# Kernel tuning notes

Measured on AMD Instinct MI355X. Metric: run time of the kernel, lower is better.

Reference implementation:

```python
import jax, jax.numpy as jnp
import numpy as np

C_S = 768
C_Z = 128
D = 32            # c_hidden (hardcoded in module)
H = C_S // D      # 24 heads
EPS = 1e-5
INF = 1e9


def setup_inputs() -> dict:
    key = jax.random.key(0)
    ks = jax.random.split(key, 16)
    B, S = 2, 1024
    n = lambda k, shp, s=1.0: jax.random.normal(k, shp, dtype=jnp.float32) * s
    return {
        "bs": n(ks[0], (B, S, C_S)),
        "z": n(ks[1], (S, S, C_Z)),
        "t": n(ks[2], (B, C_S)),
        "beta": n(ks[3], (B, S, S), 0.1),
        "z_mask": jax.random.randint(ks[4], (S, S), 0, 2).astype(jnp.int32),
        "w_adaln": n(ks[5], (C_S, 3 * C_S), 0.02),
        "b_adaln": n(ks[6], (3 * C_S,), 0.1),
        "ln_z_w": jnp.ones((C_Z,), jnp.float32),
        "ln_z_b": jnp.zeros((C_Z,), jnp.float32),
        "w_q": n(ks[7], (C_S, C_S), 0.02),
        "w_k": n(ks[8], (C_S, C_S), 0.02),
        "w_v": n(ks[9], (C_S, C_S), 0.02),
        "w_z": n(ks[10], (C_Z, H), 0.02),
        "rms_q_w": jnp.ones((D,), jnp.float32),
        "rms_k_w": jnp.ones((D,), jnp.float32),
        "w_o": n(ks[11], (C_S, C_S), 0.02),
        "b_o": jnp.zeros((C_S,), jnp.float32),
    }


def _ln(x, eps=EPS):
    mu = jnp.mean(x, axis=-1, keepdims=True)
    var = jnp.mean((x - mu) ** 2, axis=-1, keepdims=True)
    return (x - mu) * jax.lax.rsqrt(var + eps)


def _rms(x, w, eps=EPS):
    return x * jax.lax.rsqrt(jnp.mean(x * x, axis=-1, keepdims=True) + eps) * w


def reference(bs, z, t, beta, z_mask, w_adaln, b_adaln, ln_z_w, ln_z_b,
              w_q, w_k, w_v, w_z, rms_q_w, rms_k_w, w_o, b_o):
    B, S, _ = bs.shape
    # AdaLayerNormZero: SiLU(t) -> Linear -> (shift, scale, gate)
    emb = jax.nn.silu(t) @ w_adaln + b_adaln                # [B, 3*C_S]
    shift, scale, gate = jnp.split(emb, 3, axis=-1)
    bs_norm = _ln(bs) * (1.0 + scale[:, None, :]) + shift[:, None, :]
    gate = gate[:, None, :]                                  # [B,1,C_S]
    # LayerNorm on pair rep
    z_norm = _ln(z) * ln_z_w + ln_z_b                        # [S,S,C_Z]
    # Q/K/V with QK-RMSNorm
    q = _rms((bs_norm @ w_q).reshape(B, S, H, D).transpose(0, 2, 1, 3), rms_q_w)
    k = _rms((bs_norm @ w_k).reshape(B, S, H, D).transpose(0, 2, 1, 3), rms_k_w)
    v = (bs_norm @ w_v).reshape(B, S, H, D).transpose(0, 2, 1, 3)
    # pair bias [1,H,S,S] + mask bias + beta
    bias = jnp.einsum('ijc,ch->hij', z_norm, w_z)[None]
    mask_bias = jnp.where(z_mask.astype(jnp.float32) > 0.5, 0.0, -INF)[None, None]
    bias = bias + mask_bias + beta[:, None, :, :]
    scores = jnp.einsum('bhqd,bhkd->bhqk', q, k) * (1.0 / np.sqrt(D)) + bias
    attn = jax.nn.softmax(scores, axis=-1)
    out = jnp.einsum('bhqk,bhkd->bhqd', attn, v).transpose(0, 2, 1, 3).reshape(B, S, C_S)
    return (out @ w_o + b_o) * gate
```

## Files before the change

### kernel.cpp

```cpp
#include <hip/hip_runtime.h>
#include <hip/hip_bf16.h>
#include <math.h>

#define SQ 1024
#define CS 768
#define CZ 128
#define DD 32
#define NH 24
#define EPSV 1e-5f

typedef __hip_bfloat16 bf16;
typedef _Float16 f16;
typedef _Float16 f16x8 __attribute__((ext_vector_type(8)));
typedef float f32x4 __attribute__((ext_vector_type(4)));

__device__ __forceinline__ float b2f(bf16 x) { return __bfloat162float(x); }
__device__ __forceinline__ bf16 f2b(float x) { return __float2bfloat16(x); }

__global__ __launch_bounds__(256) void k_adaln(const float* t, const float* w,
                                               const float* bias, float* emb) {
    __shared__ float st[CS];
    int b = blockIdx.y;
    int o = blockIdx.x * 256 + threadIdx.x;
    for (int c = threadIdx.x; c < CS; c += 256) {
        float x = t[b * CS + c];
        st[c] = x / (1.0f + __expf(-x));
    }
    __syncthreads();
    float acc = bias[o];
    for (int c = 0; c < CS; ++c)
        acc += st[c] * w[(size_t)c * (3 * CS) + o];
    emb[(size_t)b * 3 * CS + o] = acc;
}

__global__ __launch_bounds__(256) void k_bsnorm(const float* bs, const float* emb,
                                                float* bsn) {
    int row = blockIdx.x;
    int b = row >> 10;
    const float* x = bs + (size_t)row * CS;
    float v[3], s1 = 0.f, s2 = 0.f;
    #pragma unroll
    for (int i = 0; i < 3; i++) {
        float f = x[threadIdx.x + i * 256];
        v[i] = f; s1 += f; s2 += f * f;
    }
    __shared__ float red[8];
    for (int off = 32; off; off >>= 1) { s1 += __shfl_down(s1, off); s2 += __shfl_down(s2, off); }
    int wid = threadIdx.x >> 6;
    if ((threadIdx.x & 63) == 0) { red[wid] = s1; red[wid + 4] = s2; }
    __syncthreads();
    s1 = red[0] + red[1] + red[2] + red[3];
    s2 = red[4] + red[5] + red[6] + red[7];
    float mu = s1 * (1.0f / CS);
    float var = s2 * (1.0f / CS) - mu * mu;
    float rs = rsqrtf(var + EPSV);
    const float* sh = emb + (size_t)b * 3 * CS;
    float* o = bsn + (size_t)row * CS;
    #pragma unroll
    for (int i = 0; i < 3; i++) {
        int c = threadIdx.x + i * 256;
        o[c] = (v[i] - mu) * rs * (1.0f + sh[CS + c]) + sh[c];
    }
}

__global__ __launch_bounds__(256) void k_gemm_qkv(const float* A, const float* W,
                                                  float* out) {
    __shared__ float As[16][68];
    __shared__ float Bs[16][68];
    int t = threadIdx.x;
    int m0g = blockIdx.x * 64;
    int n0g = blockIdx.y * 64;
    int mg = t >> 4, ng = t & 15;
    float acc[4][4] = {};
    for (int k0 = 0; k0 < CS; k0 += 16) {
        {
            int kk = t & 15, mm = t >> 4;
            #pragma unroll
            for (int r = 0; r < 4; r++)
                As[kk][mm + r * 16] = A[(size_t)(m0g + mm + r * 16) * CS + k0 + kk];
            int nn = (t & 15) * 4, kb = t >> 4;
            float4 w4 = *(const float4*)&W[(size_t)(k0 + kb) * CS + n0g + nn];
            *(float4*)&Bs[kb][nn] = w4;
        }
        __syncthreads();
        #pragma unroll
        for (int kk = 0; kk < 16; kk++) {
            float4 a4 = *(const float4*)&As[kk][mg * 4];
            float4 b4 = *(const float4*)&Bs[kk][ng * 4];
            float a[4] = {a4.x, a4.y, a4.z, a4.w};
            float bv[4] = {b4.x, b4.y, b4.z, b4.w};
            #pragma unroll
            for (int ii = 0; ii < 4; ii++)
                #pragma unroll
                for (int jj = 0; jj < 4; jj++)
                    acc[ii][jj] += a[ii] * bv[jj];
        }
        __syncthreads();
    }
    #pragma unroll
    for (int ii = 0; ii < 4; ii++) {
        int r = m0g + mg * 4 + ii;
        int b = r >> 10, s = r & 1023;
        #pragma unroll
        for (int jj = 0; jj < 4; jj++) {
            int c = n0g + ng * 4 + jj;
            int h = c >> 5, d = c & 31;
            out[(((size_t)b * NH + h) * SQ + s) * DD + d] = acc[ii][jj];
        }
    }
}

__global__ __launch_bounds__(256) void k_rms(float* x, const float* w) {
    int g = blockIdx.x * 8 + (threadIdx.x >> 5);
    int d = threadIdx.x & 31;
    float* p = x + (size_t)g * DD + d;
    float v = *p;
    float s = v * v;
    for (int off = 16; off; off >>= 1) s += __shfl_xor(s, off, 32);
    float rs = rsqrtf(s * (1.0f / DD) + EPSV);
    *p = v * rs * w[d];
}

__global__ __launch_bounds__(64) void k_uv(const float* wz, const float* lnw,
                                           const float* lnb, float* uv) {
    int t = threadIdx.x;
    if (t < 2 * NH) {
        int h = t % NH;
        const float* s = (t < NH) ? lnw : lnb;
        float a = 0.f;
        for (int c = 0; c < CZ; ++c) a += s[c] * wz[c * NH + h];
        uv[t] = a;
    }
}

#define ZROWS 64
#define ZSTRIDE 132
__global__ __launch_bounds__(256) void k_zbias(const float* z, const int* zmask,
                                               const float* wz, const float* lnw,
                                               const float* lnb, const float* uv,
                                               bf16* zbias) {
    __shared__ float zt[ZROWS * ZSTRIDE];
    __shared__ bf16 ot[NH][ZROWS];
    int t = threadIdx.x;
    size_t base = (size_t)blockIdx.x * ZROWS;
    const float4* src = (const float4*)(z + base * CZ);
    #pragma unroll
    for (int it = 0; it < 8; it++) {
        int gi = t + it * 256;
        int row = gi >> 5, c4 = gi & 31;
        int cs = (c4 * 4) ^ ((row >> 3) << 2);
        *(float4*)&zt[row * ZSTRIDE + cs] = src[gi];
    }
    __syncthreads();
    int lane = t & 63;
    int qd = __builtin_amdgcn_readfirstlane(t >> 6);
    int sw = (lane >> 3) << 2;
    float acc[NH];
    #pragma unroll
    for (int h = 0; h < NH; h++) acc[h] = 0.f;
    float s1 = 0.f, s2 = 0.f;
    #pragma unroll
    for (int i = 0; i < 8; i++) {
        int c0 = qd * 32 + i * 4;
        float4 zv = *(const float4*)&zt[lane * ZSTRIDE + (c0 ^ sw)];
        float e[4] = {zv.x, zv.y, zv.z, zv.w};
        #pragma unroll
        for (int u = 0; u < 4; u++) {
            int c = c0 + u;
            float zval = e[u];
            s1 += zval;
            s2 = fmaf(zval, zval, s2);
            float tc = zval * lnw[c];
            #pragma unroll
            for (int h = 0; h < NH; h++)
                acc[h] = fmaf(tc, wz[c * NH + h], acc[h]);
        }
    }
    __syncthreads();
    {
        float* pp = zt + qd * (ZROWS * 27) + lane * 27;
        pp[0] = s1; pp[1] = s2;
        #pragma unroll
        for (int h = 0; h < NH; h++) pp[2 + h] = acc[h];
    }
    __syncthreads();
    int r = lane;
    int hb = qd * 6;
    float fs1 = 0.f, fs2 = 0.f;
    float fa[6] = {};
    #pragma unroll
    for (int q = 0; q < 4; q++) {
        const float* p = zt + q * (ZROWS * 27) + r * 27;
        fs1 += p[0]; fs2 += p[1];
        #pragma unroll
        for (int j = 0; j < 6; j++) fa[j] += p[2 + hb + j];
    }
    float mu = fs1 * (1.0f / CZ);
    float var = fs2 * (1.0f / CZ) - mu * mu;
    float rs = rsqrtf(var + EPSV);
    float mb = (zmask[base + r] > 0) ? 0.0f : -1.0e9f;
    #pragma unroll
    for (int j = 0; j < 6; j++) {
        int h = hb + j;
        float val = rs * fa[j] - mu * rs * uv[h] + uv[NH + h] + mb;
        ot[h][r] = f2b(val);
    }
    __syncthreads();
    size_t SS = (size_t)SQ * SQ;
    if (t < 192) {
        int h = t >> 3, l8 = t & 7;
        uint4 val = *(const uint4*)&ot[h][l8 * 8];
        *(uint4*)&zbias[(size_t)h * SS + base + l8 * 8] = val;
    }
}

#define PQK 40
#define PPV 72
__global__ __launch_bounds__(256) void k_attn(const float* q, const float* k,
                                              const float* v, const bf16* zbias,
                                              const float* beta, float* attn_out) {
    int qt = blockIdx.x;
    int bh = blockIdx.y;
    int b = bh / NH, h = bh % NH;
    __shared__ f16 Qs[64 * PQK];
    __shared__ f16 Ks[64 * PQK];
    __shared__ f16 Vs[32 * PPV];
    __shared__ f16 Ps[64 * PPV];
    int t = threadIdx.x;
    int w = t >> 6, l = t & 63;
    int lg = l >> 4, ll = l & 15;
    const float scale = 0.17677669529663687f;
    size_t SS = (size_t)SQ * SQ;
    int srow = t >> 2, sc0 = (t & 3) * 8;

    {
        const float* qb = q + ((size_t)bh * SQ + qt * 64) * DD;
        float4 a0 = *(const float4*)&qb[srow * DD + sc0];
        float4 a1 = *(const float4*)&qb[srow * DD + sc0 + 4];
        f16x8 hv;
        hv[0] = (f16)(a0.x * scale); hv[1] = (f16)(a0.y * scale);
        hv[2] = (f16)(a0.z * scale); hv[3] = (f16)(a0.w * scale);
        hv[4] = (f16)(a1.x * scale); hv[5] = (f16)(a1.y * scale);
        hv[6] = (f16)(a1.z * scale); hv[7] = (f16)(a1.w * scale);
        *(f16x8*)&Qs[srow * PQK + sc0] = hv;
    }
    f32x4 accO0 = {0.f, 0.f, 0.f, 0.f}, accO1 = {0.f, 0.f, 0.f, 0.f};
    float m_reg[4], l_reg[4];
    #pragma unroll
    for (int r = 0; r < 4; r++) { m_reg[r] = -3.0e38f; l_reg[r] = 0.f; }

    float4 kr0, kr1, vr0, vr1;
    {
        const float* kb = k + ((size_t)bh * SQ) * DD;
        const float* vb = v + ((size_t)bh * SQ) * DD;
        kr0 = *(const float4*)&kb[srow * DD + sc0];
        kr1 = *(const float4*)&kb[srow * DD + sc0 + 4];
        vr0 = *(const float4*)&vb[srow * DD + sc0];
        vr1 = *(const float4*)&vb[srow * DD + sc0 + 4];
    }
    __syncthreads();
    {
        f16x8 hk;
        hk[0] = (f16)kr0.x; hk[1] = (f16)kr0.y; hk[2] = (f16)kr0.z; hk[3] = (f16)kr0.w;
        hk[4] = (f16)kr1.x; hk[5] = (f16)kr1.y; hk[6] = (f16)kr1.z; hk[7] = (f16)kr1.w;
        *(f16x8*)&Ks[srow * PQK + sc0] = hk;
        float vv[8] = {vr0.x, vr0.y, vr0.z, vr0.w, vr1.x, vr1.y, vr1.z, vr1.w};
        #pragma unroll
        for (int u = 0; u < 8; u++) Vs[(sc0 + u) * PPV + srow] = (f16)vv[u];
    }
    const unsigned short* zb = (const unsigned short*)(zbias + (size_t)h * SS);
    const float* bb = beta + (size_t)b * SS;
    int ibase = qt * 64 + w * 16 + lg * 4;

    for (int kt = 0; kt < 16; kt++) {
        __syncthreads();
        if (kt < 15) {
            const float* kb = k + ((size_t)bh * SQ + (kt + 1) * 64) * DD;
            const float* vb = v + ((size_t)bh * SQ + (kt + 1) * 64) * DD;
            kr0 = *(const float4*)&kb[srow * DD + sc0];
            kr1 = *(const float4*)&kb[srow * DD + sc0 + 4];
            vr0 = *(const float4*)&vb[srow * DD + sc0];
            vr1 = *(const float4*)&vb[srow * DD + sc0 + 4];
        }
        f32x4 acc[4];
        #pragma unroll
        for (int c = 0; c < 4; c++) {
            #pragma unroll
            for (int r = 0; r < 4; r++) {
                size_t off = (size_t)(ibase + r) * SQ + kt * 64 + c * 16 + ll;
                union { unsigned u; float f; } cv;
                cv.u = (unsigned)zb[off] << 16;
                acc[c][r] = cv.f + bb[off];
            }
        }
        f16x8 aQ = *(const f16x8*)&Qs[(w * 16 + ll) * PQK + lg * 8];
        #pragma unroll
        for (int c = 0; c < 4; c++) {
            f16x8 bK = *(const f16x8*)&Ks[(c * 16 + ll) * PQK + lg * 8];
            acc[c] = __builtin_amdgcn_mfma_f32_16x16x32_f16(aQ, bK, acc[c], 0, 0, 0);
        }
        float al[4];
        #pragma unroll
        for (int r = 0; r < 4; r++) {
            float mx = fmaxf(fmaxf(acc[0][r], acc[1][r]), fmaxf(acc[2][r], acc[3][r]));
            #pragma unroll
            for (int off = 1; off < 16; off <<= 1) mx = fmaxf(mx, __shfl_xor(mx, off, 64));
            float mn = fmaxf(m_reg[r], mx);
            al[r] = __expf(m_reg[r] - mn);
            float ps = 0.f;
            #pragma unroll
            for (int c = 0; c < 4; c++) {
                float p = __expf(acc[c][r] - mn);
                acc[c][r] = p;
                ps += p;
            }
            #pragma unroll
            for (int off = 1; off < 16; off <<= 1) ps += __shfl_xor(ps, off, 64);
            m_reg[r] = mn;
            l_reg[r] = l_reg[r] * al[r] + ps;
        }
        #pragma unroll
        for (int c = 0; c < 4; c++)
            #pragma unroll
            for (int r = 0; r < 4; r++)
                Ps[(w * 16 + lg * 4 + r) * PPV + c * 16 + ll] = (f16)acc[c][r];
        #pragma unroll
        for (int r = 0; r < 4; r++) { accO0[r] *= al[r]; accO1[r] *= al[r]; }
        __asm__ volatile("s_waitcnt lgkmcnt(0)" ::: "memory");
        #pragma unroll
        for (int jt = 0; jt < 2; jt++) {
            f16x8 aP = *(const f16x8*)&Ps[(w * 16 + ll) * PPV + jt * 32 + lg * 8];
            f16x8 bV0 = *(const f16x8*)&Vs[(ll) * PPV + jt * 32 + lg * 8];
            f16x8 bV1 = *(const f16x8*)&Vs[(16 + ll) * PPV + jt * 32 + lg * 8];
            accO0 = __builtin_amdgcn_mfma_f32_16x16x32_f16(aP, bV0, accO0, 0, 0, 0);
            accO1 = __builtin_amdgcn_mfma_f32_16x16x32_f16(aP, bV1, accO1, 0, 0, 0);
        }
        __syncthreads();
        if (kt < 15) {
            f16x8 hk;
            hk[0] = (f16)kr0.x; hk[1] = (f16)kr0.y; hk[2] = (f16)kr0.z; hk[3] = (f16)kr0.w;
            hk[4] = (f16)kr1.x; hk[5] = (f16)kr1.y; hk[6] = (f16)kr1.z; hk[7] = (f16)kr1.w;
            *(f16x8*)&Ks[srow * PQK + sc0] = hk;
            float vv[8] = {vr0.x, vr0.y, vr0.z, vr0.w, vr1.x, vr1.y, vr1.z, vr1.w};
            #pragma unroll
            for (int u = 0; u < 8; u++) Vs[(sc0 + u) * PPV + srow] = (f16)vv[u];
        }
    }
    #pragma unroll
    for (int r = 0; r < 4; r++) {
        float inv = 1.0f / l_reg[r];
        int row = qt * 64 + w * 16 + lg * 4 + r;
        float* op = attn_out + ((size_t)b * SQ + row) * CS + h * DD;
        op[ll] = accO0[r] * inv;
        op[16 + ll] = accO1[r] * inv;
    }
}

__global__ __launch_bounds__(256) void k_gemm_out(const float* A, const float* W,
                                                  const float* b_o, const float* emb,
                                                  float* out) {
    __shared__ float As[16][68];
    __shared__ float Bs[16][68];
    int t = threadIdx.x;
    int m0g = blockIdx.x * 64;
    int n0g = blockIdx.y * 64;
    int mg = t >> 4, ng = t & 15;
    float acc[4][4] = {};
    for (int k0 = 0; k0 < CS; k0 += 16) {
        {
            int kk = t & 15, mm = t >> 4;
            #pragma unroll
            for (int r = 0; r < 4; r++)
                As[kk][mm + r * 16] = A[(size_t)(m0g + mm + r * 16) * CS + k0 + kk];
            int nn = (t & 15) * 4, kb = t >> 4;
            float4 w4 = *(const float4*)&W[(size_t)(k0 + kb) * CS + n0g + nn];
            *(float4*)&Bs[kb][nn] = w4;
        }
        __syncthreads();
        #pragma unroll
        for (int kk = 0; kk < 16; kk++) {
            float4 a4 = *(const float4*)&As[kk][mg * 4];
            float4 b4 = *(const float4*)&Bs[kk][ng * 4];
            float a[4] = {a4.x, a4.y, a4.z, a4.w};
            float bv[4] = {b4.x, b4.y, b4.z, b4.w};
            #pragma unroll
            for (int ii = 0; ii < 4; ii++)
                #pragma unroll
                for (int jj = 0; jj < 4; jj++)
                    acc[ii][jj] += a[ii] * bv[jj];
        }
        __syncthreads();
    }
    #pragma unroll
    for (int ii = 0; ii < 4; ii++) {
        int r = m0g + mg * 4 + ii;
        int b = r >> 10;
        int c0 = n0g + ng * 4;
        const float* gt = emb + (size_t)b * 3 * CS + 2 * CS;
        float4 o4;
        o4.x = (acc[ii][0] + b_o[c0 + 0]) * gt[c0 + 0];
        o4.y = (acc[ii][1] + b_o[c0 + 1]) * gt[c0 + 1];
        o4.z = (acc[ii][2] + b_o[c0 + 2]) * gt[c0 + 2];
        o4.w = (acc[ii][3] + b_o[c0 + 3]) * gt[c0 + 3];
        *(float4*)&out[(size_t)r * CS + c0] = o4;
    }
}

extern "C" void kernel_launch(void* const* d_in, const int* in_sizes, int n_in,
                              void* d_out, int out_size, void* d_ws, size_t ws_size,
                              hipStream_t stream) {
    const float* bs      = (const float*)d_in[0];
    const float* z       = (const float*)d_in[1];
    const float* t       = (const float*)d_in[2];
    const float* beta    = (const float*)d_in[3];
    const int*   z_mask  = (const int*)d_in[4];
    const float* w_adaln = (const float*)d_in[5];
    const float* b_adaln = (const float*)d_in[6];
    const float* ln_z_w  = (const float*)d_in[7];
    const float* ln_z_b  = (const float*)d_in[8];
    const float* w_q     = (const float*)d_in[9];
    const float* w_k     = (const float*)d_in[10];
    const float* w_v     = (const float*)d_in[11];
    const float* w_z     = (const float*)d_in[12];
    const float* rms_q_w = (const float*)d_in[13];
    const float* rms_k_w = (const float*)d_in[14];
    const float* w_o     = (const float*)d_in[15];
    const float* b_o     = (const float*)d_in[16];
    float* out = (float*)d_out;

    char* ws = (char*)d_ws;
    const size_t SZ_QKV = (size_t)2 * SQ * CS * 4;
    float* emb   = (float*)(ws);
    float* bsn   = (float*)(ws + 32768);
    float* qbuf  = (float*)(ws + 32768 + SZ_QKV);
    float* kbuf  = (float*)(ws + 32768 + 2 * SZ_QKV);
    float* vbuf  = (float*)(ws + 32768 + 3 * SZ_QKV);
    float* attn  = (float*)(ws + 32768 + 4 * SZ_QKV);
    bf16*  zbias = (bf16*)(ws + 32768 + 5 * SZ_QKV);
    float* uv    = (float*)(ws + 32768 + 5 * SZ_QKV + 50331648);

    k_adaln<<<dim3(9, 2), 256, 0, stream>>>(t, w_adaln, b_adaln, emb);
    k_uv<<<1, 64, 0, stream>>>(w_z, ln_z_w, ln_z_b, uv);
    k_bsnorm<<<2048, 256, 0, stream>>>(bs, emb, bsn);
    k_gemm_qkv<<<dim3(32, 12), 256, 0, stream>>>(bsn, w_q, qbuf);
    k_gemm_qkv<<<dim3(32, 12), 256, 0, stream>>>(bsn, w_k, kbuf);
    k_gemm_qkv<<<dim3(32, 12), 256, 0, stream>>>(bsn, w_v, vbuf);
    k_rms<<<6144, 256, 0, stream>>>(qbuf, rms_q_w);
    k_rms<<<6144, 256, 0, stream>>>(kbuf, rms_k_w);
    k_zbias<<<16384, 256, 0, stream>>>(z, z_mask, w_z, ln_z_w, ln_z_b, uv, zbias);
    k_attn<<<dim3(16, 48), 256, 0, stream>>>(qbuf, kbuf, vbuf, zbias, beta, attn);
    k_gemm_out<<<dim3(32, 12), 256, 0, stream>>>(attn, w_o, b_o, emb, out);
}
```

Baseline: 1.108 ms.

## Move QKV and output projections to fp16 MFMA GEMMs with fused RMSNorm

Replaces the fp32 scalar SIMT GEMMs with a templated fp16 MFMA GEMM, 128x64 tile. Weights are transposed and cast to fp16 by a new per-call kernel, and bs_norm and the attention output are now stored as fp16. The three QKV GEMMs are merged into one launch using the z grid dimension, and the QK RMSNorm is fused into the GEMM epilogue through lane shuffles, removing the two separate k_rms passes. The aim is to cut GEMM compute time and intermediate memory traffic. The cost is lower input precision on the projections and an extra weight-conversion kernel on every call.

```diff
diff --git a/kernel.cpp b/kernel.cpp
--- a/kernel.cpp
+++ b/kernel.cpp
@@ -12,6 +12,7 @@
 typedef __hip_bfloat16 bf16;
 typedef _Float16 f16;
 typedef _Float16 f16x8 __attribute__((ext_vector_type(8)));
+typedef _Float16 f16x4 __attribute__((ext_vector_type(4)));
 typedef float f32x4 __attribute__((ext_vector_type(4)));
 
 __device__ __forceinline__ float b2f(bf16 x) { return __bfloat162float(x); }
@@ -34,7 +35,7 @@
 }
 
 __global__ __launch_bounds__(256) void k_bsnorm(const float* bs, const float* emb,
-                                                float* bsn) {
+                                                f16* bsn) {
     int row = blockIdx.x;
     int b = row >> 10;
     const float* x = bs + (size_t)row * CS;
@@ -55,70 +56,113 @@
     float var = s2 * (1.0f / CS) - mu * mu;
     float rs = rsqrtf(var + EPSV);
     const float* sh = emb + (size_t)b * 3 * CS;
-    float* o = bsn + (size_t)row * CS;
+    f16* o = bsn + (size_t)row * CS;
     #pragma unroll
     for (int i = 0; i < 3; i++) {
         int c = threadIdx.x + i * 256;
-        o[c] = (v[i] - mu) * rs * (1.0f + sh[CS + c]) + sh[c];
-    }
-}
-
-__global__ __launch_bounds__(256) void k_gemm_qkv(const float* A, const float* W,
-                                                  float* out) {
-    __shared__ float As[16][68];
-    __shared__ float Bs[16][68];
+        o[c] = (f16)((v[i] - mu) * rs * (1.0f + sh[CS + c]) + sh[c]);
+    }
+}
+
+__global__ __launch_bounds__(256) void k_wt(const float* wq, const float* wk,
+                                            const float* wv, const float* wo,
+                                            f16* wt) {
+    int z = blockIdx.z;
+    const float* W = (z == 0) ? wq : (z == 1) ? wk : (z == 2) ? wv : wo;
+    f16* WT = wt + (size_t)z * CS * CS;
+    __shared__ float ts[64][68];
     int t = threadIdx.x;
-    int m0g = blockIdx.x * 64;
-    int n0g = blockIdx.y * 64;
-    int mg = t >> 4, ng = t & 15;
-    float acc[4][4] = {};
-    for (int k0 = 0; k0 < CS; k0 += 16) {
-        {
-            int kk = t & 15, mm = t >> 4;
-            #pragma unroll
-            for (int r = 0; r < 4; r++)
-                As[kk][mm + r * 16] = A[(size_t)(m0g + mm + r * 16) * CS + k0 + kk];
-            int nn = (t & 15) * 4, kb = t >> 4;
-            float4 w4 = *(const float4*)&W[(size_t)(k0 + kb) * CS + n0g + nn];
-            *(float4*)&Bs[kb][nn] = w4;
-        }
+    int k0 = blockIdx.x * 64, n0 = blockIdx.y * 64;
+    #pragma unroll
+    for (int i = 0; i < 4; i++) {
+        int kr = (t >> 4) + i * 16, nc = (t & 15) * 4;
+        float4 v4 = *(const float4*)&W[(size_t)(k0 + kr) * CS + n0 + nc];
+        ts[kr][nc] = v4.x; ts[kr][nc + 1] = v4.y;
+        ts[kr][nc + 2] = v4.z; ts[kr][nc + 3] = v4.w;
+    }
+    __syncthreads();
+    #pragma unroll
+    for (int i = 0; i < 4; i++) {
+        int nr = (t >> 4) + i * 16, kc = (t & 15) * 4;
+        f16x4 h4;
+        h4[0] = (f16)ts[kc][nr]; h4[1] = (f16)ts[kc + 1][nr];
+        h4[2] = (f16)ts[kc + 2][nr]; h4[3] = (f16)ts[kc + 3][nr];
+        *(f16x4*)&WT[(size_t)(n0 + nr) * CS + k0 + kc] = h4;
+    }
+}
+
+#define GP 40
+template<int MODE>
+__global__ __launch_bounds__(256) void k_gemm16(const f16* A, const f16* WT,
+                                                float* out, const float* rwq,
+                                                const float* rwk, const float* b_o,
+                                                const float* emb) {
+    __shared__ f16 As[128 * GP];
+    __shared__ f16 Ws[64 * GP];
+    int t = threadIdx.x;
+    int m0 = blockIdx.x * 128, n0 = blockIdx.y * 64;
+    int z = blockIdx.z;
+    const f16* Ab = A + (size_t)m0 * CS;
+    const f16* Wb = WT + (size_t)z * CS * CS + (size_t)n0 * CS;
+    if (MODE == 0) out += (size_t)z * ((size_t)2 * SQ * CS);
+    int w = t >> 6, l = t & 63;
+    int lg = l >> 4, ll = l & 15;
+    int wr = w >> 1, wc = w & 1;
+    int sr = t >> 2, sk = (t & 3) * 8;
+    f32x4 acc[4][2] = {};
+    for (int k0 = 0; k0 < CS; k0 += 32) {
+        #pragma unroll
+        for (int it = 0; it < 2; it++) {
+            int r = sr + it * 64;
+            *(f16x8*)&As[r * GP + sk] = *(const f16x8*)&Ab[(size_t)r * CS + k0 + sk];
+        }
+        *(f16x8*)&Ws[sr * GP + sk] = *(const f16x8*)&Wb[(size_t)sr * CS + k0 + sk];
         __syncthreads();
-        #pragma unroll
-        for (int kk = 0; kk < 16; kk++) {
-            float4 a4 = *(const float4*)&As[kk][mg * 4];
-            float4 b4 = *(const float4*)&Bs[kk][ng * 4];
-            float a[4] = {a4.x, a4.y, a4.z, a4.w};
-            float bv[4] = {b4.x, b4.y, b4.z, b4.w};
-            #pragma unroll
-            for (int ii = 0; ii < 4; ii++)
-                #pragma unroll
-                for (int jj = 0; jj < 4; jj++)
-                    acc[ii][jj] += a[ii] * bv[jj];
-        }
+        f16x8 af[4], bf[2];
+        #pragma unroll
+        for (int mi = 0; mi < 4; mi++)
+            af[mi] = *(const f16x8*)&As[(wr * 64 + mi * 16 + ll) * GP + lg * 8];
+        #pragma unroll
+        for (int ni = 0; ni < 2; ni++)
+            bf[ni] = *(const f16x8*)&Ws[(wc * 32 + ni * 16 + ll) * GP + lg * 8];
+        #pragma unroll
+        for (int mi = 0; mi < 4; mi++)
+            #pragma unroll
+            for (int ni = 0; ni < 2; ni++)
+                acc[mi][ni] = __builtin_amdgcn_mfma_f32_16x16x32_f16(
+                    af[mi], bf[ni], acc[mi][ni], 0, 0, 0);
         __syncthreads();
     }
-    #pragma unroll
-    for (int ii = 0; ii < 4; ii++) {
-        int r = m0g + mg * 4 + ii;
-        int b = r >> 10, s = r & 1023;
-        #pragma unroll
-        for (int jj = 0; jj < 4; jj++) {
-            int c = n0g + ng * 4 + jj;
-            int h = c >> 5, d = c & 31;
-            out[(((size_t)b * NH + h) * SQ + s) * DD + d] = acc[ii][jj];
-        }
-    }
-}
-
-__global__ __launch_bounds__(256) void k_rms(float* x, const float* w) {
-    int g = blockIdx.x * 8 + (threadIdx.x >> 5);
-    int d = threadIdx.x & 31;
-    float* p = x + (size_t)g * DD + d;
-    float v = *p;
-    float s = v * v;
-    for (int off = 16; off; off >>= 1) s += __shfl_xor(s, off, 32);
-    float rs = rsqrtf(s * (1.0f / DD) + EPSV);
-    *p = v * rs * w[d];
+    int c0 = n0 + wc * 32;
+    const float* rw = (z == 0) ? rwq : rwk;
+    #pragma unroll
+    for (int mi = 0; mi < 4; mi++) {
+        #pragma unroll
+        for (int rg = 0; rg < 4; rg++) {
+            int r = m0 + wr * 64 + mi * 16 + lg * 4 + rg;
+            int bb = r >> 10, s = r & 1023;
+            float v0 = acc[mi][0][rg], v1 = acc[mi][1][rg];
+            if (MODE == 0) {
+                if (z < 2) {
+                    float sq = v0 * v0 + v1 * v1;
+                    sq += __shfl_xor(sq, 1); sq += __shfl_xor(sq, 2);
+                    sq += __shfl_xor(sq, 4); sq += __shfl_xor(sq, 8);
+                    float rs = rsqrtf(sq * (1.0f / DD) + EPSV);
+                    v0 *= rs * rw[ll];
+                    v1 *= rs * rw[16 + ll];
+                }
+                int h = c0 >> 5;
+                float* op = out + (((size_t)bb * NH + h) * SQ + s) * DD;
+                op[ll] = v0;
+                op[16 + ll] = v1;
+            } else {
+                const float* gt = emb + (size_t)bb * 3 * CS + 2 * CS;
+                out[(size_t)r * CS + c0 + ll] = (v0 + b_o[c0 + ll]) * gt[c0 + ll];
+                out[(size_t)r * CS + c0 + 16 + ll] =
+                    (v1 + b_o[c0 + 16 + ll]) * gt[c0 + 16 + ll];
+            }
+        }
+    }
 }
 
 __global__ __launch_bounds__(64) void k_uv(const float* wz, const float* lnw,
@@ -218,7 +262,7 @@
 #define PPV 72
 __global__ __launch_bounds__(256) void k_attn(const float* q, const float* k,
                                               const float* v, const bf16* zbias,
-                                              const float* beta, float* attn_out) {
+                                              const float* beta, f16* attn_out) {
     int qt = blockIdx.x;
     int bh = blockIdx.y;
     int b = bh / NH, h = bh % NH;
@@ -350,59 +394,9 @@
     for (int r = 0; r < 4; r++) {
         float inv = 1.0f / l_reg[r];
         int row = qt * 64 + w * 16 + lg * 4 + r;
-        float* op = attn_out + ((size_t)b * SQ + row) * CS + h * DD;
-        op[ll] = accO0[r] * inv;
-        op[16 + ll] = accO1[r] * inv;
-    }
-}
-
-__global__ __launch_bounds__(256) void k_gemm_out(const float* A, const float* W,
-                                                  const float* b_o, const float* emb,
-                                                  float* out) {
-    __shared__ float As[16][68];
-    __shared__ float Bs[16][68];
-    int t = threadIdx.x;
-    int m0g = blockIdx.x * 64;
-    int n0g = blockIdx.y * 64;
-    int mg = t >> 4, ng = t & 15;
-    float acc[4][4] = {};
-    for (int k0 = 0; k0 < CS; k0 += 16) {
-        {
-            int kk = t & 15, mm = t >> 4;
-            #pragma unroll
-            for (int r = 0; r < 4; r++)
-                As[kk][mm + r * 16] = A[(size_t)(m0g + mm + r * 16) * CS + k0 + kk];
-            int nn = (t & 15) * 4, kb = t >> 4;
-            float4 w4 = *(const float4*)&W[(size_t)(k0 + kb) * CS + n0g + nn];
-            *(float4*)&Bs[kb][nn] = w4;
-        }
-        __syncthreads();
-        #pragma unroll
-        for (int kk = 0; kk < 16; kk++) {
-            float4 a4 = *(const float4*)&As[kk][mg * 4];
-            float4 b4 = *(const float4*)&Bs[kk][ng * 4];
-            float a[4] = {a4.x, a4.y, a4.z, a4.w};
-            float bv[4] = {b4.x, b4.y, b4.z, b4.w};
-            #pragma unroll
-            for (int ii = 0; ii < 4; ii++)
-                #pragma unroll
-                for (int jj = 0; jj < 4; jj++)
-                    acc[ii][jj] += a[ii] * bv[jj];
-        }
-        __syncthreads();
-    }
-    #pragma unroll
-    for (int ii = 0; ii < 4; ii++) {
-        int r = m0g + mg * 4 + ii;
-        int b = r >> 10;
-        int c0 = n0g + ng * 4;
-        const float* gt = emb + (size_t)b * 3 * CS + 2 * CS;
-        float4 o4;
-        o4.x = (acc[ii][0] + b_o[c0 + 0]) * gt[c0 + 0];
-        o4.y = (acc[ii][1] + b_o[c0 + 1]) * gt[c0 + 1];
-        o4.z = (acc[ii][2] + b_o[c0 + 2]) * gt[c0 + 2];
-        o4.w = (acc[ii][3] + b_o[c0 + 3]) * gt[c0 + 3];
-        *(float4*)&out[(size_t)r * CS + c0] = o4;
+        f16* op = attn_out + ((size_t)b * SQ + row) * CS + h * DD;
+        op[ll] = (f16)(accO0[r] * inv);
+        op[16 + ll] = (f16)(accO1[r] * inv);
     }
 }
 
@@ -431,23 +425,23 @@
     char* ws = (char*)d_ws;
     const size_t SZ_QKV = (size_t)2 * SQ * CS * 4;
     float* emb   = (float*)(ws);
-    float* bsn   = (float*)(ws + 32768);
+    f16*   bsn   = (f16*)(ws + 32768);
     float* qbuf  = (float*)(ws + 32768 + SZ_QKV);
     float* kbuf  = (float*)(ws + 32768 + 2 * SZ_QKV);
     float* vbuf  = (float*)(ws + 32768 + 3 * SZ_QKV);
-    float* attn  = (float*)(ws + 32768 + 4 * SZ_QKV);
+    f16*   attn  = (f16*)(ws + 32768 + 4 * SZ_QKV);
     bf16*  zbias = (bf16*)(ws + 32768 + 5 * SZ_QKV);
     float* uv    = (float*)(ws + 32768 + 5 * SZ_QKV + 50331648);
+    f16*   wt    = (f16*)(ws + 32768 + 5 * SZ_QKV + 50331648 + 4096);
 
     k_adaln<<<dim3(9, 2), 256, 0, stream>>>(t, w_adaln, b_adaln, emb);
     k_uv<<<1, 64, 0, stream>>>(w_z, ln_z_w, ln_z_b, uv);
+    k_wt<<<dim3(12, 12, 4), 256, 0, stream>>>(w_q, w_k, w_v, w_o, wt);
     k_bsnorm<<<2048, 256, 0, stream>>>(bs, emb, bsn);
-    k_gemm_qkv<<<dim3(32, 12), 256, 0, stream>>>(bsn, w_q, qbuf);
-    k_gemm_qkv<<<dim3(32, 12), 256, 0, stream>>>(bsn, w_k, kbuf);
-    k_gemm_qkv<<<dim3(32, 12), 256, 0, stream>>>(bsn, w_v, vbuf);
-    k_rms<<<6144, 256, 0, stream>>>(qbuf, rms_q_w);
-    k_rms<<<6144, 256, 0, stream>>>(kbuf, rms_k_w);
+    k_gemm16<0><<<dim3(16, 12, 3), 256, 0, stream>>>(bsn, wt, qbuf, rms_q_w,
+                                                     rms_k_w, nullptr, nullptr);
     k_zbias<<<16384, 256, 0, stream>>>(z, z_mask, w_z, ln_z_w, ln_z_b, uv, zbias);
     k_attn<<<dim3(16, 48), 256, 0, stream>>>(qbuf, kbuf, vbuf, zbias, beta, attn);
-    k_gemm_out<<<dim3(32, 12), 256, 0, stream>>>(attn, w_o, b_o, emb, out);
-}
+    k_gemm16<1><<<dim3(16, 12, 1), 256, 0, stream>>>(attn, wt + (size_t)3 * CS * CS,
+                                                     out, nullptr, nullptr, b_o, emb);
+}
```

After: 920.6 us. -16.9%, faster.
